# Performance work log

Hardware: AMD Instinct MI355X
Metric: run time of the kernel (lower is better)

## Reference

```python
import jax, jax.numpy as jnp
import numpy as np

DIM = 256


def setup_inputs() -> dict:
    key = jax.random.key(0)
    ks = jax.random.split(key, 10)
    d = DIM
    inp = {
        "agent": jax.random.normal(ks[0], (64, d), dtype=jnp.float32),
        "x": jax.random.normal(ks[1], (8, 4096, d), dtype=jnp.float32),
        # parameters (stored as [in, out]; y = x @ W + b)
        "W_qkv": jax.random.normal(ks[2], (d, 3 * d), dtype=jnp.float32) * (d ** -0.5),
        "b_qkv": jnp.zeros((3 * d,), dtype=jnp.float32),
        "W_agent": jax.random.normal(ks[3], (d, 2 * d), dtype=jnp.float32) * (d ** -0.5),
        "b_agent": jnp.zeros((2 * d,), dtype=jnp.float32),
        "W_fc1": jax.random.normal(ks[4], (d, d), dtype=jnp.float32) * (d ** -0.5),
        "b_fc1": jnp.zeros((d,), dtype=jnp.float32),
        "W_fc2": jax.random.normal(ks[5], (d, d), dtype=jnp.float32) * (d ** -0.5),
        "b_fc2": jnp.zeros((d,), dtype=jnp.float32),
    }
    return inp


def reference(agent, x, W_qkv, b_qkv, W_agent, b_agent, W_fc1, b_fc1, W_fc2, b_fc2):
    d = x.shape[-1]
    scale = d ** -0.5
    # qkv projection of tokens: [B,N,3d] -> q,k,v each [B,N,d]
    qkv = x @ W_qkv + b_qkv
    q, k, v = jnp.split(qkv, 3, axis=-1)
    # agent projection: [K,2d] -> q_agent,k_agent each [K,d]
    ag = agent @ W_agent + b_agent
    q_agent, k_agent = jnp.split(ag, 2, axis=-1)
    # stage 1: agents attend over tokens -> [B,K,N]
    attn1 = jax.nn.softmax(jnp.einsum('kd,bnd->bkn', q_agent, k) * scale, axis=-1)
    va = jnp.einsum('bkn,bnd->bkd', attn1, v)  # [B,K,d]
    va = va @ W_fc1 + b_fc1
    # stage 2: tokens attend over agents -> [B,N,K]
    attn2 = jax.nn.softmax(jnp.einsum('bnd,kd->bnk', q, k_agent) * scale, axis=-1)
    out = jnp.einsum('bnk,bkd->bnd', attn2, va)  # [B,N,d]
    out = out @ W_fc2 + b_fc2
    return out + x
```

## Files before the change

### kernel.cpp

```cpp
#include <hip/hip_runtime.h>
#include <stdint.h>
#include <string.h>

#define BB 8
#define NN 4096
#define DD 256
#define SCALE 0.0625f
#define XS 264
#define XT 72

using frag_ab = __attribute__((ext_vector_type(8))) short;
using frag_cd = __attribute__((ext_vector_type(4))) float;

__device__ __forceinline__ unsigned short f2bf(float f) {
    union { float f; unsigned u; } a; a.f = f;
    unsigned r = a.u + 0x7FFFu + ((a.u >> 16) & 1u);
    return (unsigned short)(r >> 16);
}
__device__ __forceinline__ float bf2f(unsigned short h) {
    union { unsigned u; float f; } a; a.u = ((unsigned)h) << 16;
    return a.f;
}

__global__ __launch_bounds__(256) void k_setup(
    const float* __restrict__ agent, const float* __restrict__ Wag,
    const float* __restrict__ bag, const float* __restrict__ Wqkv,
    const float* __restrict__ bqkv, const float* __restrict__ Wfc1,
    const float* __restrict__ bfc1, const float* __restrict__ Wfc2,
    unsigned short* __restrict__ P12t, float* __restrict__ c2,
    unsigned short* __restrict__ W3b, float* __restrict__ b3)
{
    __shared__ float arow[256];
    __shared__ float red[256];
    const int bx = blockIdx.x, tid = threadIdx.x;
    if (bx < 128) {
        const int c = bx;
        const int woff = (c < 64) ? 256 : 0;
        const int aoff = (c < 64) ? 0 : 256;
        const int row = c & 63;
        float s = bag[aoff + tid];
        for (int o = 0; o < 256; ++o) s += agent[row * 256 + o] * Wag[o * 512 + aoff + tid];
        arow[tid] = s;
        __syncthreads();
        float p = 0.f;
        for (int o = 0; o < 256; ++o) p += Wqkv[tid * 768 + woff + o] * arow[o];
        P12t[(size_t)c * 256 + tid] = f2bf(SCALE * p);
        if (c >= 64) {
            red[tid] = bqkv[woff + tid] * arow[tid];
            __syncthreads();
            for (int st = 128; st; st >>= 1) {
                if (tid < st) red[tid] += red[tid + st];
                __syncthreads();
            }
            if (tid == 0) c2[c - 64] = SCALE * red[0];
        }
    } else if (bx < 384) {
        const int i = bx - 128;
        float t = 0.f;
        for (int o = 0; o < 256; ++o) t += Wqkv[i * 768 + 512 + o] * Wfc1[o * 256 + tid];
        arow[tid] = t;
        __syncthreads();
        float p = 0.f;
        for (int k = 0; k < 256; ++k) p += arow[k] * Wfc2[k * 256 + tid];
        W3b[(size_t)i * 256 + tid] = f2bf(p);
    } else {
        float t = bfc1[tid];
        for (int o = 0; o < 256; ++o) t += bqkv[512 + o] * Wfc1[o * 256 + tid];
        arow[tid] = t;
        __syncthreads();
        float p = 0.f;
        for (int k = 0; k < 256; ++k) p += arow[k] * Wfc2[k * 256 + tid];
        b3[tid] = p;
    }
}

__global__ __launch_bounds__(256) void k_fuse(
    const float* __restrict__ x, const unsigned short* __restrict__ P12t,
    const float* __restrict__ c2, unsigned short* __restrict__ p2b,
    unsigned short* __restrict__ part, float* __restrict__ statS)
{
    __shared__ unsigned short xtile[64 * XS];
    __shared__ unsigned short Bs[128 * XT];
    __shared__ unsigned short Pl[64 * XT];
    __shared__ float Ss[4][64];
    const int s = blockIdx.x, b = blockIdx.y;
    const int n0 = s * 64;
    const int tid = threadIdx.x;
    const int w = tid >> 6, lane = tid & 63;
    const int ml = lane & 15, q = lane >> 4;

#pragma unroll
    for (int p = 0; p < 16; ++p) {
        int idx = p * 256 + tid;
        int tok = idx >> 6, d = (idx & 63) * 4;
        float4 v = *(const float4*)&x[(size_t)(b * 4096 + n0 + tok) * 256 + d];
        unsigned short u[4] = {f2bf(v.x), f2bf(v.y), f2bf(v.z), f2bf(v.w)};
        uint2 pk; memcpy(&pk, u, 8);
        *(uint2*)&xtile[tok * XS + d] = pk;
    }
    __syncthreads();

    frag_cd acc1[8];
#pragma unroll
    for (int j = 0; j < 8; ++j)
#pragma unroll
        for (int r = 0; r < 4; ++r) acc1[j][r] = 0.f;

    for (int kb = 0; kb < 256; kb += 64) {
        __syncthreads();
#pragma unroll
        for (int p = 0; p < 4; ++p) {
            int idx = p * 256 + tid;
            int r = idx >> 3, c = (idx & 7) * 8;
            *(uint4*)&Bs[r * XT + c] = *(const uint4*)&P12t[(size_t)r * 256 + kb + c];
        }
        __syncthreads();
#pragma unroll
        for (int ks = 0; ks < 2; ++ks) {
            const int kk = ks * 32 + q * 8;
            frag_ab a = *(const frag_ab*)&xtile[(w * 16 + ml) * XS + kb + kk];
#pragma unroll
            for (int j = 0; j < 8; ++j) {
                frag_ab bf = *(const frag_ab*)&Bs[(j * 16 + ml) * XT + kk];
                acc1[j] = __builtin_amdgcn_mfma_f32_16x16x32_bf16(a, bf, acc1[j], 0, 0, 0);
            }
        }
    }

    {
        float cc[4];
#pragma unroll
        for (int j = 0; j < 4; ++j) cc[j] = c2[j * 16 + ml];
#pragma unroll
        for (int r = 0; r < 4; ++r) {
            float e[4], sum = 0.f;
#pragma unroll
            for (int j = 0; j < 4; ++j) {
                e[j] = __expf(acc1[4 + j][r] + cc[j]);
                sum += e[j];
            }
#pragma unroll
            for (int mask = 1; mask <= 8; mask <<= 1) sum += __shfl_xor(sum, mask);
            float inv = 1.f / sum;
            const int tok = n0 + w * 16 + q * 4 + r;
#pragma unroll
            for (int j = 0; j < 4; ++j)
                p2b[(size_t)(b * 4096 + tok) * 64 + j * 16 + ml] = f2bf(e[j] * inv);
        }
    }

    float e1[4][4];
#pragma unroll
    for (int j = 0; j < 4; ++j) {
#pragma unroll
        for (int r = 0; r < 4; ++r) e1[j][r] = __expf(acc1[j][r]);
        float sj = e1[j][0] + e1[j][1] + e1[j][2] + e1[j][3];
        sj += __shfl_xor(sj, 16);
        sj += __shfl_xor(sj, 32);
        if (lane < 16) Ss[w][j * 16 + ml] = sj;
    }

#pragma unroll
    for (int j = 0; j < 4; ++j)
#pragma unroll
        for (int r = 0; r < 4; ++r)
            Pl[(j * 16 + ml) * XT + w * 16 + q * 4 + r] = f2bf(e1[j][r]);
    __syncthreads();

    if (tid < 64)
        statS[(size_t)(b * 64 + tid) * 64 + s] =
            Ss[0][tid] + Ss[1][tid] + Ss[2][tid] + Ss[3][tid];

    frag_cd acc2[4][4];
#pragma unroll
    for (int af = 0; af < 4; ++af)
#pragma unroll
        for (int i = 0; i < 4; ++i)
#pragma unroll
            for (int r = 0; r < 4; ++r) acc2[af][i][r] = 0.f;
#pragma unroll
    for (int ks = 0; ks < 2; ++ks) {
        const int kk = ks * 32 + q * 8;
        frag_ab a[4], bf[4];
#pragma unroll
        for (int af = 0; af < 4; ++af)
            a[af] = *(const frag_ab*)&Pl[(af * 16 + ml) * XT + kk];
#pragma unroll
        for (int i = 0; i < 4; ++i) {
            const int d = w * 64 + i * 16 + ml;
            unsigned short u[8];
#pragma unroll
            for (int t = 0; t < 8; ++t) u[t] = xtile[(kk + t) * XS + d];
            memcpy(&bf[i], u, 16);
        }
#pragma unroll
        for (int af = 0; af < 4; ++af)
#pragma unroll
            for (int i = 0; i < 4; ++i)
                acc2[af][i] = __builtin_amdgcn_mfma_f32_16x16x32_bf16(
                    a[af], bf[i], acc2[af][i], 0, 0, 0);
    }
#pragma unroll
    for (int af = 0; af < 4; ++af)
#pragma unroll
        for (int i = 0; i < 4; ++i)
#pragma unroll
            for (int r = 0; r < 4; ++r)
                part[(size_t)((s * 8 + b) * 64 + af * 16 + q * 4 + r) * 256 +
                     w * 64 + i * 16 + ml] = f2bf(acc2[af][i][r]);
}

__global__ __launch_bounds__(256) void k_fc(
    const unsigned short* __restrict__ part, const float* __restrict__ statS,
    const unsigned short* __restrict__ W3b, const float* __restrict__ b3,
    unsigned short* __restrict__ va3t)
{
    __shared__ float rowb[256];
    __shared__ float rs[64];
    const int row = blockIdx.x, tid = threadIdx.x;
    const int b = row >> 6, agc = row & 63;
    if (tid < 64) rs[tid] = statS[(size_t)(b * 64 + agc) * 64 + tid];
    float sv = 0.f;
    for (int s = 0; s < 64; ++s)
        sv += bf2f(part[(size_t)((s * 8 + b) * 64 + agc) * 256 + tid]);
    __syncthreads();
    float tot = 0.f;
#pragma unroll
    for (int t = 0; t < 64; ++t) tot += rs[t];
    rowb[tid] = sv / tot;
    __syncthreads();
    float s2 = b3[tid];
    for (int k = 0; k < 256; ++k) s2 += rowb[k] * bf2f(W3b[(size_t)k * 256 + tid]);
    va3t[(size_t)(b * 256 + tid) * 64 + agc] = f2bf(s2);
}

__global__ __launch_bounds__(256) void k_stage2(
    const unsigned short* __restrict__ p2b, const unsigned short* __restrict__ va3t,
    const float* __restrict__ x, const float* __restrict__ bfc2,
    float* __restrict__ out)
{
    __shared__ unsigned short Vs[256 * 72];
    __shared__ unsigned short Ps[64 * 72];
    const int n0 = blockIdx.x * 64, b = blockIdx.y;
    const int tid = threadIdx.x;
    const int w = tid >> 6, lane = tid & 63;
    const int ml = lane & 15, q = lane >> 4;

#pragma unroll
    for (int p = 0; p < 8; ++p) {
        int idx = p * 256 + tid;
        int r = idx >> 3, c = (idx & 7) * 8;
        *(uint4*)&Vs[r * 72 + c] = *(const uint4*)&va3t[(size_t)(b * 256 + r) * 64 + c];
    }
#pragma unroll
    for (int p = 0; p < 2; ++p) {
        int idx = p * 256 + tid;
        int r = idx >> 3, c = (idx & 7) * 8;
        *(uint4*)&Ps[r * 72 + c] = *(const uint4*)&p2b[(size_t)(b * 4096 + n0 + r) * 64 + c];
    }
    __syncthreads();

    frag_cd acc[4][4];
#pragma unroll
    for (int i = 0; i < 4; ++i)
#pragma unroll
        for (int j = 0; j < 4; ++j)
#pragma unroll
            for (int r = 0; r < 4; ++r) acc[i][j][r] = 0.f;
#pragma unroll
    for (int ks = 0; ks < 2; ++ks) {
        const int kk = ks * 32 + q * 8;
        frag_ab a[4], bf[4];
#pragma unroll
        for (int i = 0; i < 4; ++i)
            a[i] = *(const frag_ab*)&Vs[(w * 64 + i * 16 + ml) * 72 + kk];
#pragma unroll
        for (int j = 0; j < 4; ++j)
            bf[j] = *(const frag_ab*)&Ps[(j * 16 + ml) * 72 + kk];
#pragma unroll
        for (int i = 0; i < 4; ++i)
#pragma unroll
            for (int j = 0; j < 4; ++j)
                acc[i][j] = __builtin_amdgcn_mfma_f32_16x16x32_bf16(
                    a[i], bf[j], acc[i][j], 0, 0, 0);
    }

#pragma unroll
    for (int i = 0; i < 4; ++i) {
        const int d0 = w * 64 + i * 16 + q * 4;
        float4 bias = *(const float4*)&bfc2[d0];
#pragma unroll
        for (int j = 0; j < 4; ++j) {
            const int tok = n0 + j * 16 + ml;
            size_t ad = (size_t)(b * 4096 + tok) * 256 + d0;
            float4 xr = *(const float4*)&x[ad];
            float4 o;
            o.x = acc[i][j][0] + bias.x + xr.x;
            o.y = acc[i][j][1] + bias.y + xr.y;
            o.z = acc[i][j][2] + bias.z + xr.z;
            o.w = acc[i][j][3] + bias.w + xr.w;
            *(float4*)&out[ad] = o;
        }
    }
}

extern "C" void kernel_launch(void* const* d_in, const int* in_sizes, int n_in,
                              void* d_out, int out_size, void* d_ws, size_t ws_size,
                              hipStream_t stream) {
    const float* agent = (const float*)d_in[0];
    const float* x     = (const float*)d_in[1];
    const float* Wqkv  = (const float*)d_in[2];
    const float* bqkv  = (const float*)d_in[3];
    const float* Wag   = (const float*)d_in[4];
    const float* bag   = (const float*)d_in[5];
    const float* Wfc1  = (const float*)d_in[6];
    const float* bfc1  = (const float*)d_in[7];
    const float* Wfc2  = (const float*)d_in[8];
    const float* bfc2  = (const float*)d_in[9];
    float* out = (float*)d_out;

    char* w = (char*)d_ws;
    size_t off = 0;
    unsigned short* p2b  = (unsigned short*)(w + off); off += (size_t)BB * NN * 64 * 2;
    unsigned short* part = (unsigned short*)(w + off); off += (size_t)64 * BB * 64 * 256 * 2;
    float* statS = (float*)(w + off); off += (size_t)BB * 64 * 64 * 4;
    unsigned short* P12t = (unsigned short*)(w + off); off += (size_t)128 * 256 * 2;
    float* c2   = (float*)(w + off); off += 256 * 4;
    unsigned short* W3b = (unsigned short*)(w + off); off += (size_t)256 * 256 * 2;
    float* b3   = (float*)(w + off); off += 256 * 4;
    unsigned short* va3t = (unsigned short*)(w + off); off += (size_t)BB * DD * 64 * 2;

    k_setup<<<385, 256, 0, stream>>>(agent, Wag, bag, Wqkv, bqkv, Wfc1, bfc1, Wfc2,
                                     P12t, c2, W3b, b3);
    k_fuse<<<dim3(64, BB), 256, 0, stream>>>(x, P12t, c2, p2b, part, statS);
    k_fc<<<512, 256, 0, stream>>>(part, statS, W3b, b3, va3t);
    k_stage2<<<dim3(64, BB), 256, 0, stream>>>(p2b, va3t, x, bfc2, out);
}
```

Measured before the change: 160.9 us.

## Accumulate stage-1 partials with float atomics and coalesce setup weight reads

Stage-1 per-slice partial sums (64 slices of bf16 [B,64,256]) and softmax row sums are no longer written to a large scratch buffer and re-reduced in k_fc. They are now atomically accumulated in fp32 into a small zeroed buffer, with a memset added before launch. k_setup's projection loop now uses wave-level coalesced row reads with shuffle reductions instead of strided per-thread reads, and k_fuse register-prefetches the next P12t tile. The atomics add contention and non-deterministic summation order.

```diff
diff --git a/kernel.cpp b/kernel.cpp
--- a/kernel.cpp
+++ b/kernel.cpp
@@ -33,18 +33,29 @@
     __shared__ float arow[256];
     __shared__ float red[256];
     const int bx = blockIdx.x, tid = threadIdx.x;
+    const int w = tid >> 6, lane = tid & 63;
     if (bx < 128) {
         const int c = bx;
         const int woff = (c < 64) ? 256 : 0;
         const int aoff = (c < 64) ? 0 : 256;
         const int row = c & 63;
         float s = bag[aoff + tid];
-        for (int o = 0; o < 256; ++o) s += agent[row * 256 + o] * Wag[o * 512 + aoff + tid];
+        for (int o = 0; o < 256; ++o)
+            s += agent[row * 256 + o] * Wag[o * 512 + aoff + tid];
         arow[tid] = s;
         __syncthreads();
-        float p = 0.f;
-        for (int o = 0; o < 256; ++o) p += Wqkv[tid * 768 + woff + o] * arow[o];
-        P12t[(size_t)c * 256 + tid] = f2bf(SCALE * p);
+        for (int i0 = 0; i0 < 64; ++i0) {
+            const int i = w * 64 + i0;
+            const float* wr = &Wqkv[(size_t)i * 768 + woff];
+            float partial = wr[lane] * arow[lane]
+                          + wr[64 + lane] * arow[64 + lane]
+                          + wr[128 + lane] * arow[128 + lane]
+                          + wr[192 + lane] * arow[192 + lane];
+#pragma unroll
+            for (int mask = 32; mask; mask >>= 1)
+                partial += __shfl_xor(partial, mask);
+            if (lane == 0) P12t[(size_t)c * 256 + i] = f2bf(SCALE * partial);
+        }
         if (c >= 64) {
             red[tid] = bqkv[woff + tid] * arow[tid];
             __syncthreads();
@@ -57,7 +68,8 @@
     } else if (bx < 384) {
         const int i = bx - 128;
         float t = 0.f;
-        for (int o = 0; o < 256; ++o) t += Wqkv[i * 768 + 512 + o] * Wfc1[o * 256 + tid];
+        for (int o = 0; o < 256; ++o)
+            t += Wqkv[i * 768 + 512 + o] * Wfc1[o * 256 + tid];
         arow[tid] = t;
         __syncthreads();
         float p = 0.f;
@@ -77,7 +89,7 @@
 __global__ __launch_bounds__(256) void k_fuse(
     const float* __restrict__ x, const unsigned short* __restrict__ P12t,
     const float* __restrict__ c2, unsigned short* __restrict__ p2b,
-    unsigned short* __restrict__ part, float* __restrict__ statS)
+    float* __restrict__ va_acc, float* __restrict__ statR)
 {
     __shared__ unsigned short xtile[64 * XS];
     __shared__ unsigned short Bs[128 * XT];
@@ -106,13 +118,29 @@
 #pragma unroll
         for (int r = 0; r < 4; ++r) acc1[j][r] = 0.f;
 
-    for (int kb = 0; kb < 256; kb += 64) {
+    uint4 pre[4];
+#pragma unroll
+    for (int p = 0; p < 4; ++p) {
+        int idx = p * 256 + tid;
+        int r = idx >> 3, c = (idx & 7) * 8;
+        pre[p] = *(const uint4*)&P12t[(size_t)r * 256 + c];
+    }
+    for (int kbi = 0; kbi < 4; ++kbi) {
+        const int kb = kbi * 64;
         __syncthreads();
 #pragma unroll
         for (int p = 0; p < 4; ++p) {
             int idx = p * 256 + tid;
             int r = idx >> 3, c = (idx & 7) * 8;
-            *(uint4*)&Bs[r * XT + c] = *(const uint4*)&P12t[(size_t)r * 256 + kb + c];
+            *(uint4*)&Bs[r * XT + c] = pre[p];
+        }
+        if (kbi < 3) {
+#pragma unroll
+            for (int p = 0; p < 4; ++p) {
+                int idx = p * 256 + tid;
+                int r = idx >> 3, c = (idx & 7) * 8;
+                pre[p] = *(const uint4*)&P12t[(size_t)r * 256 + kb + 64 + c];
+            }
         }
         __syncthreads();
 #pragma unroll
@@ -168,8 +196,8 @@
     __syncthreads();
 
     if (tid < 64)
-        statS[(size_t)(b * 64 + tid) * 64 + s] =
-            Ss[0][tid] + Ss[1][tid] + Ss[2][tid] + Ss[3][tid];
+        atomicAdd(&statR[b * 64 + tid],
+                  Ss[0][tid] + Ss[1][tid] + Ss[2][tid] + Ss[3][tid]);
 
     frag_cd acc2[4][4];
 #pragma unroll
@@ -206,28 +234,21 @@
         for (int i = 0; i < 4; ++i)
 #pragma unroll
             for (int r = 0; r < 4; ++r)
-                part[(size_t)((s * 8 + b) * 64 + af * 16 + q * 4 + r) * 256 +
-                     w * 64 + i * 16 + ml] = f2bf(acc2[af][i][r]);
+                atomicAdd(&va_acc[(size_t)(b * 64 + af * 16 + q * 4 + r) * 256 +
+                                  w * 64 + i * 16 + ml],
+                          acc2[af][i][r]);
 }
 
 __global__ __launch_bounds__(256) void k_fc(
-    const unsigned short* __restrict__ part, const float* __restrict__ statS,
+    const float* __restrict__ va_acc, const float* __restrict__ statR,
     const unsigned short* __restrict__ W3b, const float* __restrict__ b3,
     unsigned short* __restrict__ va3t)
 {
     __shared__ float rowb[256];
-    __shared__ float rs[64];
     const int row = blockIdx.x, tid = threadIdx.x;
     const int b = row >> 6, agc = row & 63;
-    if (tid < 64) rs[tid] = statS[(size_t)(b * 64 + agc) * 64 + tid];
-    float sv = 0.f;
-    for (int s = 0; s < 64; ++s)
-        sv += bf2f(part[(size_t)((s * 8 + b) * 64 + agc) * 256 + tid]);
-    __syncthreads();
-    float tot = 0.f;
-#pragma unroll
-    for (int t = 0; t < 64; ++t) tot += rs[t];
-    rowb[tid] = sv / tot;
+    const float inv = 1.f / statR[b * 64 + agc];
+    rowb[tid] = va_acc[(size_t)(b * 64 + agc) * 256 + tid] * inv;
     __syncthreads();
     float s2 = b3[tid];
     for (int k = 0; k < 256; ++k) s2 += rowb[k] * bf2f(W3b[(size_t)k * 256 + tid]);
@@ -319,20 +340,22 @@
     const float* bfc2  = (const float*)d_in[9];
     float* out = (float*)d_out;
 
-    char* w = (char*)d_ws;
+    char* wsp = (char*)d_ws;
     size_t off = 0;
-    unsigned short* p2b  = (unsigned short*)(w + off); off += (size_t)BB * NN * 64 * 2;
-    unsigned short* part = (unsigned short*)(w + off); off += (size_t)64 * BB * 64 * 256 * 2;
-    float* statS = (float*)(w + off); off += (size_t)BB * 64 * 64 * 4;
-    unsigned short* P12t = (unsigned short*)(w + off); off += (size_t)128 * 256 * 2;
-    float* c2   = (float*)(w + off); off += 256 * 4;
-    unsigned short* W3b = (unsigned short*)(w + off); off += (size_t)256 * 256 * 2;
-    float* b3   = (float*)(w + off); off += 256 * 4;
-    unsigned short* va3t = (unsigned short*)(w + off); off += (size_t)BB * DD * 64 * 2;
+    unsigned short* p2b = (unsigned short*)(wsp + off); off += (size_t)BB * NN * 64 * 2;
+    float* va_acc = (float*)(wsp + off); off += (size_t)BB * 64 * 256 * 4;
+    float* statR  = (float*)(wsp + off); off += (size_t)BB * 64 * 4;
+    unsigned short* P12t = (unsigned short*)(wsp + off); off += (size_t)128 * 256 * 2;
+    float* c2   = (float*)(wsp + off); off += 256 * 4;
+    unsigned short* W3b = (unsigned short*)(wsp + off); off += (size_t)256 * 256 * 2;
+    float* b3   = (float*)(wsp + off); off += 256 * 4;
+    unsigned short* va3t = (unsigned short*)(wsp + off); off += (size_t)BB * DD * 64 * 2;
+
+    hipMemsetAsync(va_acc, 0, (size_t)BB * 64 * 256 * 4 + (size_t)BB * 64 * 4, stream);
 
     k_setup<<<385, 256, 0, stream>>>(agent, Wag, bag, Wqkv, bqkv, Wfc1, bfc1, Wfc2,
                                      P12t, c2, W3b, b3);
-    k_fuse<<<dim3(64, BB), 256, 0, stream>>>(x, P12t, c2, p2b, part, statS);
-    k_fc<<<512, 256, 0, stream>>>(part, statS, W3b, b3, va3t);
+    k_fuse<<<dim3(64, BB), 256, 0, stream>>>(x, P12t, c2, p2b, va_acc, statR);
+    k_fc<<<512, 256, 0, stream>>>(va_acc, statR, W3b, b3, va3t);
     k_stage2<<<dim3(64, BB), 256, 0, stream>>>(p2b, va3t, x, bfc2, out);
 }
```

Result: slower. 203.2 us (+26.3%).
